# Kernel optimization log

Hardware: AMD Instinct MI355X
Metric: run time of the kernel (lower is better)

The kernel has to match this reference:

```python
import jax, jax.numpy as jnp
import numpy as np

# pywt db4 reconstruction low-pass (rec_lo) coefficients.
_H = np.array([
    0.23037781330885523, 0.7148465705525415, 0.6308807679295904,
    -0.02798376941698385, -0.18703481171888114, 0.030841381835986965,
    0.032883011666982945, -0.010597401784997278], dtype=np.float64)
# pywt dec_lo = _H[::-1]; conv (flipped) correlation kernel = dec_lo[::-1] = _H.
_FLO = _H
# dec_hi[k] = (-1)^(7-k) * _H[k]; correlation kernel = dec_hi[::-1] -> (-1)^k * _H[7-k].
_FHI = np.array([(-1.0) ** k * _H[7 - k] for k in range(8)])
_FILT = jnp.asarray(np.stack([_FLO, _FHI])[:, None, :], dtype=jnp.float32)  # [2,1,8]
_PAD = 7  # filter_len - 1
_LEVEL = 4


def _dwt_step(sig):
    """One pywt dwt level, mode='symmetric'. sig: [N, L] -> (cA, cD), each [N, (L+7)//2]."""
    # symmetric (half-sample) extension by filter_len-1 each side, drop first sample
    # so that stride-2 VALID correlation reproduces pywt's output phase/length.
    xp = jnp.pad(sig, ((0, 0), (_PAD, _PAD)), mode='symmetric')[:, 1:]
    out = jax.lax.conv_general_dilated(
        xp[:, None, :], _FILT, window_strides=(2,), padding='VALID',
        dimension_numbers=('NCH', 'OIH', 'NCH'))  # [N, 2, (L+7)//2]
    return out[:, 0, :], out[:, 1, :]


def setup_inputs() -> dict:
    key = jax.random.key(0)
    x = jax.random.normal(key, (64, 4096, 32), dtype=jnp.float32)  # [B, L, C]
    return {"x": x}


def reference(x):
    """Faithful batched version of pywt.wavedec(x[i,:,j], 'db4', 'symmetric', level=4).
    Returns tuple (cA4, cD4, cD3, cD2, cD1), each [B, C, scale_len]."""
    B, L, C = x.shape
    sig = jnp.transpose(x, (0, 2, 1)).reshape(B * C, L)
    details = []
    for _ in range(_LEVEL):
        sig, cd = _dwt_step(sig)
        details.append(cd)
    coeffs = [sig] + details[::-1]  # [cA_L, cD_L, ..., cD_1] like pywt.wavedec
    return tuple(c.reshape(B, C, c.shape[-1]) for c in coeffs)
```

## Files before the change

### kernel.cpp

```cpp
#include <hip/hip_runtime.h>


#define NT 256
#define NCHB 4

#define LPX 634
#define LP1 322
#define LP2 166
#define LP3 86
#define CDP1 314
#define CDP2 154
#define CDP3 82
#define CDP4 40
#define CAP4 40

#define L0C 4096
#define L1C 2051
#define L2C 1029
#define L3C 518
#define L4C 262
#define SC 2048

#define OFF_CD4 (SC * L4C)
#define OFF_CD3 (2 * SC * L4C)
#define OFF_CD2 (OFF_CD3 + SC * L3C)
#define OFF_CD1 (OFF_CD2 + SC * L2C)

__device__ __forceinline__ void filt8(
    const float w0, const float w1, const float w2, const float w3,
    const float w4, const float w5, const float w6, const float w7,
    float& a, float& d) {
    constexpr float FLO[8] = {
        0.23037781330885523f,  0.7148465705525415f,  0.6308807679295904f,
        -0.02798376941698385f, -0.18703481171888114f, 0.030841381835986965f,
        0.032883011666982945f, -0.010597401784997278f};
    constexpr float FHI[8] = {
        -0.010597401784997278f, -0.032883011666982945f, 0.030841381835986965f,
        0.18703481171888114f,  -0.02798376941698385f,  -0.6308807679295904f,
        0.7148465705525415f,   -0.23037781330885523f};
    float a0 = FLO[0] * w0;
    a0 = fmaf(FLO[1], w1, a0); a0 = fmaf(FLO[2], w2, a0); a0 = fmaf(FLO[3], w3, a0);
    float a1 = FLO[4] * w4;
    a1 = fmaf(FLO[5], w5, a1); a1 = fmaf(FLO[6], w6, a1); a1 = fmaf(FLO[7], w7, a1);
    a = a0 + a1;
    float d0 = FHI[0] * w0;
    d0 = fmaf(FHI[1], w1, d0); d0 = fmaf(FHI[2], w2, d0); d0 = fmaf(FHI[3], w3, d0);
    float d1 = FHI[4] * w4;
    d1 = fmaf(FHI[5], w5, d1); d1 = fmaf(FHI[6], w6, d1); d1 = fmaf(FHI[7], w7, d1);
    d = d0 + d1;
}

template <int R, bool MG, bool LAST>
__device__ __forceinline__ void level_run(
    const float* __restrict__ src, int PS, int srclo,
    float* __restrict__ dst, int PD, int DL,
    int lo, int hi,
    float* __restrict__ cdbuf, int CDP,
    float* __restrict__ cabuf,
    int c, int slot) {
    static_assert((R & 1) == 0, "R must be even");
    const int span = hi - lo;
    const int nrun = span / R;
    bool tail = false;
    int i0;
    if (slot < nrun) {
        i0 = lo + slot * R;
    } else if (slot == nrun && nrun * R < span) {
        i0 = lo + ((span - R) & ~1);
        tail = (span & 1) != 0;
    } else {
        return;
    }

    const float* rowb = src + c * PS;
    const float2* row2 = reinterpret_cast<const float2*>(rowb);
    const int p = i0 - (srclo >> 1);
    float2 f0 = row2[p], f1 = row2[p + 1], f2 = row2[p + 2];

    float* dbase = LAST ? nullptr : dst + c * PD;
    float* cdbase = cdbuf + c * CDP;
    float* cabase = LAST ? cabuf + c * CAP4 : nullptr;

    float ap = 0.f, dp = 0.f;
#pragma unroll
    for (int r = 0; r < R; ++r) {
        const float2 f3 = row2[p + 3 + r];
        const int i = i0 + r;
        float a, d;
        filt8(f0.x, f0.y, f1.x, f1.y, f2.x, f2.y, f3.x, f3.y, a, d);
        if (r & 1) {
            const int w = i - 1 - lo;
            if constexpr (!LAST)
                *reinterpret_cast<float2*>(dbase + w + 6) = make_float2(ap, a);
            else
                *reinterpret_cast<float2*>(cabase + w) = make_float2(ap, a);
            *reinterpret_cast<float2*>(cdbase + w) = make_float2(dp, d);
        } else {
            ap = a; dp = d;
        }
        if constexpr (MG && !LAST) {
            if (lo == 0 && i < 6) dbase[5 - i] = a;
            if (hi == DL && i >= DL - 7) dbase[(2 * DL - 1 - i) - lo + 6] = a;
        }
        f0 = f1; f1 = f2; f2 = f3;
    }
    if (tail) {
        const int i = hi - 1;
        const float* s = rowb + 6 - srclo;
        float a, d;
        filt8(s[2*i-6], s[2*i-5], s[2*i-4], s[2*i-3],
              s[2*i-2], s[2*i-1], s[2*i],   s[2*i+1], a, d);
        if constexpr (!LAST) {
            dbase[i - lo + 6] = a;
            if constexpr (MG) {
                if (hi == DL && i >= DL - 7) dbase[(2 * DL - 1 - i) - lo + 6] = a;
            }
        } else {
            cabase[i - lo] = a;
        }
        cdbase[i - lo] = d;
    }
}

__device__ __forceinline__ void dump_rows(
    const float* __restrict__ buf, int pitch, int bufLo,
    float* __restrict__ gbase, int rowLen, int ownLo, int ownHi, int tid) {
    const int span = ownHi - ownLo;
    const int n2 = span >> 1;
    const int off = ownLo - bufLo;
#pragma unroll
    for (int c2 = 0; c2 < NCHB; ++c2) {
        const float2* s2 = reinterpret_cast<const float2*>(buf + c2 * pitch + off);
        float* g = gbase + c2 * rowLen + ownLo;
        for (int k = tid; k < n2; k += NT) {
            const float2 v = s2[k];
            g[2 * k] = v.x;
            g[2 * k + 1] = v.y;
        }
        if ((span & 1) && tid == 0) g[span - 1] = buf[c2 * pitch + off + span - 1];
    }
}

template <bool MG>
__device__ __forceinline__ void cascade(
    const float* bx, float* b1, float* b2, float* b3,
    float* cd1, float* cd2, float* cd3, float* cd4, float* ca4,
    float* __restrict__ out, int sigB, int tile, int c, int slot, int tid,
    int lox, int lo1, int hi1, int lo2, int hi2, int lo3, int hi3,
    int lo4, int hi4) {
    const int o1lo = tile ? 264 * tile - 34 : 0;
    const int o1hi = (tile == 7) ? L1C : 264 * tile + 230;
    const int o2lo = tile ? 132 * tile - 10 : 0;
    const int o2hi = (tile == 7) ? L2C : 132 * tile + 122;
    const int o3lo = tile ? 66 * tile - 2 : 0;
    const int o3hi = (tile == 7) ? L3C : 66 * tile + 64;

    level_run<6, MG, false>(bx, LPX, lox, b1, LP1, L1C, lo1, hi1, cd1, CDP1,
                            nullptr, c, slot);
    __syncthreads();

    dump_rows(cd1, CDP1, lo1, out + OFF_CD1 + sigB * L1C, L1C, o1lo, o1hi, tid);
    level_run<4, MG, false>(b1, LP1, lo1, b2, LP2, L2C, lo2, hi2, cd2, CDP2,
                            nullptr, c, slot);
    __syncthreads();

    dump_rows(cd2, CDP2, lo2, out + OFF_CD2 + sigB * L2C, L2C, o2lo, o2hi, tid);
    level_run<2, MG, false>(b2, LP2, lo2, b3, LP3, L3C, lo3, hi3, cd3, CDP3,
                            nullptr, c, slot);
    __syncthreads();

    dump_rows(cd3, CDP3, lo3, out + OFF_CD3 + sigB * L3C, L3C, o3lo, o3hi, tid);
    level_run<2, MG, true>(b3, LP3, lo3, nullptr, 0, L4C, lo4, hi4, cd4, CDP4,
                           ca4, c, slot);
    __syncthreads();

    dump_rows(cd4, CDP4, lo4, out + OFF_CD4 + sigB * L4C, L4C, lo4, hi4, tid);
    dump_rows(ca4, CAP4, lo4, out + sigB * L4C, L4C, lo4, hi4, tid);
}

__global__ __launch_bounds__(NT, 5) void fused_dwt_kernel(
    const float* __restrict__ x, float* __restrict__ out) {
    __shared__ __align__(16) float bx[NCHB * LPX];
    __shared__ __align__(16) float b1[NCHB * LP1];
    __shared__ __align__(16) float b2[NCHB * LP2];
    __shared__ __align__(16) float b3[NCHB * LP3];
    __shared__ __align__(16) float cd1[NCHB * CDP1];
    __shared__ __align__(16) float cd2[NCHB * CDP2];
    __shared__ __align__(16) float cd3[NCHB * CDP3];
    __shared__ __align__(16) float cd4[NCHB * CDP4];
    __shared__ __align__(16) float ca4[NCHB * CAP4];

    const int bid = blockIdx.x;
    const int work = (bid & 7) * 512 + (bid >> 3);
    const int cg = work & 7;
    const int tile = (work >> 3) & 7;
    const int b = work >> 6;

    const int tid = threadIdx.x;
    const int c = tid & 3;
    const int slot = tid >> 2;
    const int c0 = cg * 4;
    const int sigB = b * 32 + c0;

    const int lo4 = 33 * tile, hi4 = min(L4C, lo4 + 33);
    const int lo3 = max(0, 2 * lo4 - 6), hi3 = min(L3C, 2 * hi4);
    const int lo2 = max(0, 2 * lo3 - 6), hi2 = min(L2C, 2 * hi3);
    const int lo1 = max(0, 2 * lo2 - 6), hi1 = min(L1C, 2 * hi2);
    const int lox = max(0, 2 * lo1 - 6), hix = min(L0C, 2 * hi1);

    const float* xb = x + b * (L0C * 32) + c0;
    const int npair = (hix - lox) >> 1;
    for (int q = tid; q < npair; q += NT) {
        const int j = q << 1;
        const int t = lox + j;
        const float4 va = *reinterpret_cast<const float4*>(xb + t * 32);
        const float4 vb = *reinterpret_cast<const float4*>(xb + t * 32 + 32);
        const float av[4] = {va.x, va.y, va.z, va.w};
        const float bv[4] = {vb.x, vb.y, vb.z, vb.w};
#pragma unroll
        for (int hh = 0; hh < NCHB; ++hh)
            *reinterpret_cast<float2*>(bx + hh * LPX + 6 + j) =
                make_float2(av[hh], bv[hh]);
        if (lox == 0 && t < 6) {
#pragma unroll
            for (int hh = 0; hh < NCHB; ++hh) {
                bx[hh * LPX + 5 - t] = av[hh];
                if (t + 1 < 6) bx[hh * LPX + 4 - t] = bv[hh];
            }
        }
        if (hix == L0C && t + 1 >= L0C - 7) {
#pragma unroll
            for (int hh = 0; hh < NCHB; ++hh) {
                if (t >= L0C - 7) bx[hh * LPX + (2 * L0C - 1 - t) - lox + 6] = av[hh];
                bx[hh * LPX + (2 * L0C - 2 - t) - lox + 6] = bv[hh];
            }
        }
    }
    __syncthreads();

    if (tile == 0 || tile == 7)
        cascade<true>(bx, b1, b2, b3, cd1, cd2, cd3, cd4, ca4, out, sigB, tile,
                      c, slot, tid, lox, lo1, hi1, lo2, hi2, lo3, hi3, lo4, hi4);
    else
        cascade<false>(bx, b1, b2, b3, cd1, cd2, cd3, cd4, ca4, out, sigB, tile,
                       c, slot, tid, lox, lo1, hi1, lo2, hi2, lo3, hi3, lo4, hi4);
}

extern "C" void kernel_launch(void* const* d_in, const int* in_sizes, int n_in,
                              void* d_out, int out_size, void* d_ws, size_t ws_size,
                              hipStream_t stream) {
    (void)in_sizes; (void)n_in; (void)d_ws; (void)ws_size; (void)out_size;
    const float* x = (const float*)d_in[0];
    float* out = (float*)d_out;
    fused_dwt_kernel<<<dim3(4096), dim3(NT), 0, stream>>>(x, out);
}
```

Before: 30.11 us.

## Split fused DWT into two kernels with global workspace for levels 3-4

```diff
diff --git a/kernel.cpp b/kernel.cpp
--- a/kernel.cpp
+++ b/kernel.cpp
@@ -3,16 +3,6 @@
 
 #define NT 256
 #define NCHB 4
-
-#define LPX 634
-#define LP1 322
-#define LP2 166
-#define LP3 86
-#define CDP1 314
-#define CDP2 154
-#define CDP3 82
-#define CDP4 40
-#define CAP4 40
 
 #define L0C 4096
 #define L1C 2051
@@ -20,11 +10,23 @@
 #define L3C 518
 #define L4C 262
 #define SC 2048
+#define WSL 1032
 
 #define OFF_CD4 (SC * L4C)
 #define OFF_CD3 (2 * SC * L4C)
 #define OFF_CD2 (OFF_CD3 + SC * L3C)
 #define OFF_CD1 (OFF_CD2 + SC * L2C)
+
+#define PX1 550
+#define PB1 278
+#define PD1 266
+#define PD2 130
+#define PA2 130
+#define PAS 1042
+#define PB3 534
+#define PD3 522
+#define PD4 266
+#define PA4 266
 
 __device__ __forceinline__ void filt8(
     const float w0, const float w1, const float w2, const float w3,
@@ -56,7 +58,7 @@
     float* __restrict__ dst, int PD, int DL,
     int lo, int hi,
     float* __restrict__ cdbuf, int CDP,
-    float* __restrict__ cabuf,
+    float* __restrict__ cabuf, int CAP,
     int c, int slot) {
     static_assert((R & 1) == 0, "R must be even");
     const int span = hi - lo;
@@ -79,7 +81,7 @@
 
     float* dbase = LAST ? nullptr : dst + c * PD;
     float* cdbase = cdbuf + c * CDP;
-    float* cabase = LAST ? cabuf + c * CAP4 : nullptr;
+    float* cabase = LAST ? cabuf + c * CAP : nullptr;
 
     float ap = 0.f, dp = 0.f;
 #pragma unroll
@@ -142,53 +144,35 @@
 }
 
 template <bool MG>
-__device__ __forceinline__ void cascade(
-    const float* bx, float* b1, float* b2, float* b3,
-    float* cd1, float* cd2, float* cd3, float* cd4, float* ca4,
-    float* __restrict__ out, int sigB, int tile, int c, int slot, int tid,
-    int lox, int lo1, int hi1, int lo2, int hi2, int lo3, int hi3,
-    int lo4, int hi4) {
-    const int o1lo = tile ? 264 * tile - 34 : 0;
-    const int o1hi = (tile == 7) ? L1C : 264 * tile + 230;
-    const int o2lo = tile ? 132 * tile - 10 : 0;
-    const int o2hi = (tile == 7) ? L2C : 132 * tile + 122;
-    const int o3lo = tile ? 66 * tile - 2 : 0;
-    const int o3hi = (tile == 7) ? L3C : 66 * tile + 64;
-
-    level_run<6, MG, false>(bx, LPX, lox, b1, LP1, L1C, lo1, hi1, cd1, CDP1,
-                            nullptr, c, slot);
-    __syncthreads();
-
-    dump_rows(cd1, CDP1, lo1, out + OFF_CD1 + sigB * L1C, L1C, o1lo, o1hi, tid);
-    level_run<4, MG, false>(b1, LP1, lo1, b2, LP2, L2C, lo2, hi2, cd2, CDP2,
-                            nullptr, c, slot);
-    __syncthreads();
-
-    dump_rows(cd2, CDP2, lo2, out + OFF_CD2 + sigB * L2C, L2C, o2lo, o2hi, tid);
-    level_run<2, MG, false>(b2, LP2, lo2, b3, LP3, L3C, lo3, hi3, cd3, CDP3,
-                            nullptr, c, slot);
-    __syncthreads();
-
-    dump_rows(cd3, CDP3, lo3, out + OFF_CD3 + sigB * L3C, L3C, o3lo, o3hi, tid);
-    level_run<2, MG, true>(b3, LP3, lo3, nullptr, 0, L4C, lo4, hi4, cd4, CDP4,
-                           ca4, c, slot);
-    __syncthreads();
-
-    dump_rows(cd4, CDP4, lo4, out + OFF_CD4 + sigB * L4C, L4C, lo4, hi4, tid);
-    dump_rows(ca4, CAP4, lo4, out + sigB * L4C, L4C, lo4, hi4, tid);
-}
-
-__global__ __launch_bounds__(NT, 5) void fused_dwt_kernel(
-    const float* __restrict__ x, float* __restrict__ out) {
-    __shared__ __align__(16) float bx[NCHB * LPX];
-    __shared__ __align__(16) float b1[NCHB * LP1];
-    __shared__ __align__(16) float b2[NCHB * LP2];
-    __shared__ __align__(16) float b3[NCHB * LP3];
-    __shared__ __align__(16) float cd1[NCHB * CDP1];
-    __shared__ __align__(16) float cd2[NCHB * CDP2];
-    __shared__ __align__(16) float cd3[NCHB * CDP3];
-    __shared__ __align__(16) float cd4[NCHB * CDP4];
-    __shared__ __align__(16) float ca4[NCHB * CAP4];
+__device__ __forceinline__ void k1_cascade(
+    const float* bx, float* b1, float* cd1, float* cd2, float* ca2,
+    float* __restrict__ out, float* __restrict__ ws,
+    int sigB, int tile, int c, int slot, int tid,
+    int lox, int lo1, int hi1, int lo2, int hi2) {
+    const int o1lo = tile ? 258 * tile : 0;
+    const int o1hi = (tile == 7) ? L1C : 258 * (tile + 1);
+
+    level_run<6, MG, false>(bx, PX1, lox, b1, PB1, L1C, lo1, hi1,
+                            cd1, PD1, nullptr, 0, c, slot);
+    __syncthreads();
+
+    dump_rows(cd1, PD1, lo1, out + OFF_CD1 + sigB * L1C, L1C, o1lo, o1hi, tid);
+    level_run<4, false, true>(b1, PB1, lo1, nullptr, 0, L2C, lo2, hi2,
+                              cd2, PD2, ca2, PA2, c, slot);
+    __syncthreads();
+
+    dump_rows(cd2, PD2, lo2, out + OFF_CD2 + sigB * L2C, L2C, lo2, hi2, tid);
+    dump_rows(ca2, PA2, lo2, ws + sigB * WSL, WSL, lo2, hi2, tid);
+}
+
+__global__ __launch_bounds__(NT) void dwt12_kernel(
+    const float* __restrict__ x, float* __restrict__ out,
+    float* __restrict__ ws) {
+    __shared__ __align__(16) float bx[NCHB * PX1];
+    __shared__ __align__(16) float b1[NCHB * PB1];
+    __shared__ __align__(16) float cd1[NCHB * PD1];
+    __shared__ __align__(16) float cd2[NCHB * PD2];
+    __shared__ __align__(16) float ca2[NCHB * PA2];
 
     const int bid = blockIdx.x;
     const int work = (bid & 7) * 512 + (bid >> 3);
@@ -202,9 +186,7 @@
     const int c0 = cg * 4;
     const int sigB = b * 32 + c0;
 
-    const int lo4 = 33 * tile, hi4 = min(L4C, lo4 + 33);
-    const int lo3 = max(0, 2 * lo4 - 6), hi3 = min(L3C, 2 * hi4);
-    const int lo2 = max(0, 2 * lo3 - 6), hi2 = min(L2C, 2 * hi3);
+    const int lo2 = 129 * tile, hi2 = min(L2C, lo2 + 129);
     const int lo1 = max(0, 2 * lo2 - 6), hi1 = min(L1C, 2 * hi2);
     const int lox = max(0, 2 * lo1 - 6), hix = min(L0C, 2 * hi1);
 
@@ -219,38 +201,97 @@
         const float bv[4] = {vb.x, vb.y, vb.z, vb.w};
 #pragma unroll
         for (int hh = 0; hh < NCHB; ++hh)
-            *reinterpret_cast<float2*>(bx + hh * LPX + 6 + j) =
+            *reinterpret_cast<float2*>(bx + hh * PX1 + 6 + j) =
                 make_float2(av[hh], bv[hh]);
         if (lox == 0 && t < 6) {
 #pragma unroll
             for (int hh = 0; hh < NCHB; ++hh) {
-                bx[hh * LPX + 5 - t] = av[hh];
-                if (t + 1 < 6) bx[hh * LPX + 4 - t] = bv[hh];
+                bx[hh * PX1 + 5 - t] = av[hh];
+                if (t + 1 < 6) bx[hh * PX1 + 4 - t] = bv[hh];
             }
         }
         if (hix == L0C && t + 1 >= L0C - 7) {
 #pragma unroll
             for (int hh = 0; hh < NCHB; ++hh) {
-                if (t >= L0C - 7) bx[hh * LPX + (2 * L0C - 1 - t) - lox + 6] = av[hh];
-                bx[hh * LPX + (2 * L0C - 2 - t) - lox + 6] = bv[hh];
+                if (t >= L0C - 7) bx[hh * PX1 + (2 * L0C - 1 - t) - lox + 6] = av[hh];
+                bx[hh * PX1 + (2 * L0C - 2 - t) - lox + 6] = bv[hh];
             }
         }
     }
     __syncthreads();
 
     if (tile == 0 || tile == 7)
-        cascade<true>(bx, b1, b2, b3, cd1, cd2, cd3, cd4, ca4, out, sigB, tile,
-                      c, slot, tid, lox, lo1, hi1, lo2, hi2, lo3, hi3, lo4, hi4);
+        k1_cascade<true>(bx, b1, cd1, cd2, ca2, out, ws, sigB, tile, c, slot,
+                         tid, lox, lo1, hi1, lo2, hi2);
     else
-        cascade<false>(bx, b1, b2, b3, cd1, cd2, cd3, cd4, ca4, out, sigB, tile,
-                       c, slot, tid, lox, lo1, hi1, lo2, hi2, lo3, hi3, lo4, hi4);
+        k1_cascade<false>(bx, b1, cd1, cd2, ca2, out, ws, sigB, tile, c, slot,
+                          tid, lox, lo1, hi1, lo2, hi2);
+}
+
+__global__ __launch_bounds__(NT) void dwt34_kernel(
+    const float* __restrict__ ws, float* __restrict__ out) {
+    __shared__ __align__(16) float bA[NCHB * PAS];
+    __shared__ __align__(16) float b3[NCHB * PB3];
+    __shared__ __align__(16) float cd3[NCHB * PD3];
+    __shared__ __align__(16) float cd4[NCHB * PD4];
+    __shared__ __align__(16) float ca4[NCHB * PA4];
+
+    const int bid = blockIdx.x;
+    const int work = (bid & 7) * 64 + (bid >> 3);
+    const int cg = work & 7;
+    const int b = work >> 3;
+
+    const int tid = threadIdx.x;
+    const int c = tid & 3;
+    const int slot = tid >> 2;
+    const int sigB = b * 32 + cg * 4;
+
+    const float* wbase = ws + sigB * WSL;
+#pragma unroll
+    for (int c2 = 0; c2 < NCHB; ++c2) {
+        const float2* s2 = reinterpret_cast<const float2*>(wbase + c2 * WSL);
+        float* row = bA + c2 * PAS;
+        for (int k = tid; k < 514; k += NT) {
+            const float2 v = s2[k];
+            const int t = 2 * k;
+            *reinterpret_cast<float2*>(row + t + 6) = v;
+            if (t < 6) {
+                row[5 - t] = v.x;
+                if (t + 1 < 6) row[4 - t] = v.y;
+            }
+            if (t + 1 >= L2C - 7) {
+                if (t >= L2C - 7) row[(2 * L2C - 1 - t) + 6] = v.x;
+                row[(2 * L2C - 2 - t) + 6] = v.y;
+            }
+        }
+        if (tid == 0) {
+            const float v = wbase[c2 * WSL + (L2C - 1)];
+            row[(L2C - 1) + 6] = v;
+            row[(2 * L2C - 1 - (L2C - 1)) + 6] = v;
+        }
+    }
+    __syncthreads();
+
+    level_run<10, true, false>(bA, PAS, 0, b3, PB3, L3C, 0, L3C,
+                               cd3, PD3, nullptr, 0, c, slot);
+    __syncthreads();
+
+    dump_rows(cd3, PD3, 0, out + OFF_CD3 + sigB * L3C, L3C, 0, L3C, tid);
+    level_run<6, false, true>(b3, PB3, 0, nullptr, 0, L4C, 0, L4C,
+                              cd4, PD4, ca4, PA4, c, slot);
+    __syncthreads();
+
+    dump_rows(cd4, PD4, 0, out + OFF_CD4 + sigB * L4C, L4C, 0, L4C, tid);
+    dump_rows(ca4, PA4, 0, out + sigB * L4C, L4C, 0, L4C, tid);
 }
 
 extern "C" void kernel_launch(void* const* d_in, const int* in_sizes, int n_in,
                               void* d_out, int out_size, void* d_ws, size_t ws_size,
                               hipStream_t stream) {
-    (void)in_sizes; (void)n_in; (void)d_ws; (void)ws_size; (void)out_size;
+    (void)in_sizes; (void)n_in; (void)ws_size; (void)out_size;
     const float* x = (const float*)d_in[0];
     float* out = (float*)d_out;
-    fused_dwt_kernel<<<dim3(4096), dim3(NT), 0, stream>>>(x, out);
-}
+    float* ws = (float*)d_ws;
+    dwt12_kernel<<<dim3(4096), dim3(NT), 0, stream>>>(x, out, ws);
+    dwt34_kernel<<<dim3(512), dim3(NT), 0, stream>>>(ws, out);
+}
```

Measured after the change: 33.92 us. +12.7%, slower.

## Split each DWT level into two halves to overlap levels across barriers

Applied to the files above, without the earlier changes.

```diff
diff --git a/kernel.cpp b/kernel.cpp
--- a/kernel.cpp
+++ b/kernel.cpp
@@ -25,6 +25,11 @@
 #define OFF_CD3 (2 * SC * L4C)
 #define OFF_CD2 (OFF_CD3 + SC * L3C)
 #define OFF_CD1 (OFF_CD2 + SC * L2C)
+
+#define K1A 154
+#define K2A 72
+#define K3A 32
+#define K4A 12
 
 __device__ __forceinline__ void filt8(
     const float w0, const float w1, const float w2, const float w3,
@@ -54,9 +59,9 @@
 __device__ __forceinline__ void level_run(
     const float* __restrict__ src, int PS, int srclo,
     float* __restrict__ dst, int PD, int DL,
-    int lo, int hi,
+    int lo, int hi, int loF,
     float* __restrict__ cdbuf, int CDP,
-    float* __restrict__ cabuf,
+    float* __restrict__ cabuf, int CAP,
     int c, int slot) {
     static_assert((R & 1) == 0, "R must be even");
     const int span = hi - lo;
@@ -79,7 +84,7 @@
 
     float* dbase = LAST ? nullptr : dst + c * PD;
     float* cdbase = cdbuf + c * CDP;
-    float* cabase = LAST ? cabuf + c * CAP4 : nullptr;
+    float* cabase = LAST ? cabuf + c * CAP : nullptr;
 
     float ap = 0.f, dp = 0.f;
 #pragma unroll
@@ -89,7 +94,7 @@
         float a, d;
         filt8(f0.x, f0.y, f1.x, f1.y, f2.x, f2.y, f3.x, f3.y, a, d);
         if (r & 1) {
-            const int w = i - 1 - lo;
+            const int w = i - 1 - loF;
             if constexpr (!LAST)
                 *reinterpret_cast<float2*>(dbase + w + 6) = make_float2(ap, a);
             else
@@ -99,8 +104,8 @@
             ap = a; dp = d;
         }
         if constexpr (MG && !LAST) {
-            if (lo == 0 && i < 6) dbase[5 - i] = a;
-            if (hi == DL && i >= DL - 7) dbase[(2 * DL - 1 - i) - lo + 6] = a;
+            if (loF == 0 && i < 6) dbase[5 - i] = a;
+            if (hi == DL && i >= DL - 7) dbase[(2 * DL - 1 - i) - loF + 6] = a;
         }
         f0 = f1; f1 = f2; f2 = f3;
     }
@@ -111,14 +116,14 @@
         filt8(s[2*i-6], s[2*i-5], s[2*i-4], s[2*i-3],
               s[2*i-2], s[2*i-1], s[2*i],   s[2*i+1], a, d);
         if constexpr (!LAST) {
-            dbase[i - lo + 6] = a;
+            dbase[i - loF + 6] = a;
             if constexpr (MG) {
-                if (hi == DL && i >= DL - 7) dbase[(2 * DL - 1 - i) - lo + 6] = a;
+                if (hi == DL && i >= DL - 7) dbase[(2 * DL - 1 - i) - loF + 6] = a;
             }
         } else {
-            cabase[i - lo] = a;
-        }
-        cdbase[i - lo] = d;
+            cabase[i - loF] = a;
+        }
+        cdbase[i - loF] = d;
     }
 }
 
@@ -155,23 +160,33 @@
     const int o3lo = tile ? 66 * tile - 2 : 0;
     const int o3hi = (tile == 7) ? L3C : 66 * tile + 64;
 
-    level_run<6, MG, false>(bx, LPX, lox, b1, LP1, L1C, lo1, hi1, cd1, CDP1,
-                            nullptr, c, slot);
+    level_run<4, MG, false>(bx, LPX, lox, b1, LP1, L1C, lo1, lo1 + K1A, lo1,
+                            cd1, CDP1, nullptr, 0, c, slot);
+    __syncthreads();
+
+    level_run<4, MG, false>(bx, LPX, lox, b1, LP1, L1C, lo1 + K1A, hi1, lo1,
+                            cd1, CDP1, nullptr, 0, c, slot);
+    level_run<2, MG, false>(b1, LP1, lo1, b2, LP2, L2C, lo2, lo2 + K2A, lo2,
+                            cd2, CDP2, nullptr, 0, c, slot);
     __syncthreads();
 
     dump_rows(cd1, CDP1, lo1, out + OFF_CD1 + sigB * L1C, L1C, o1lo, o1hi, tid);
-    level_run<4, MG, false>(b1, LP1, lo1, b2, LP2, L2C, lo2, hi2, cd2, CDP2,
-                            nullptr, c, slot);
+    level_run<2, MG, false>(b1, LP1, lo1, b2, LP2, L2C, lo2 + K2A, hi2, lo2,
+                            cd2, CDP2, nullptr, 0, c, slot);
+    level_run<2, MG, false>(b2, LP2, lo2, b3, LP3, L3C, lo3, lo3 + K3A, lo3,
+                            cd3, CDP3, nullptr, 0, c, slot);
     __syncthreads();
 
     dump_rows(cd2, CDP2, lo2, out + OFF_CD2 + sigB * L2C, L2C, o2lo, o2hi, tid);
-    level_run<2, MG, false>(b2, LP2, lo2, b3, LP3, L3C, lo3, hi3, cd3, CDP3,
-                            nullptr, c, slot);
+    level_run<2, MG, false>(b2, LP2, lo2, b3, LP3, L3C, lo3 + K3A, hi3, lo3,
+                            cd3, CDP3, nullptr, 0, c, slot);
+    level_run<2, false, true>(b3, LP3, lo3, nullptr, 0, L4C, lo4, lo4 + K4A, lo4,
+                              cd4, CDP4, ca4, CAP4, c, slot);
     __syncthreads();
 
     dump_rows(cd3, CDP3, lo3, out + OFF_CD3 + sigB * L3C, L3C, o3lo, o3hi, tid);
-    level_run<2, MG, true>(b3, LP3, lo3, nullptr, 0, L4C, lo4, hi4, cd4, CDP4,
-                           ca4, c, slot);
+    level_run<2, false, true>(b3, LP3, lo3, nullptr, 0, L4C, lo4 + K4A, hi4, lo4,
+                              cd4, CDP4, ca4, CAP4, c, slot);
     __syncthreads();
 
     dump_rows(cd4, CDP4, lo4, out + OFF_CD4 + sigB * L4C, L4C, lo4, hi4, tid);
```

Result: slower. 32.32 us (+7.4%).

## Compose two DWT levels into 22-tap stride-4 filters to skip intermediate stages

Applied to the files above, without the earlier changes.

```diff
diff --git a/kernel.cpp b/kernel.cpp
--- a/kernel.cpp
+++ b/kernel.cpp
@@ -5,14 +5,12 @@
 #define NCHB 4
 
 #define LPX 634
-#define LP1 322
-#define LP2 166
-#define LP3 86
-#define CDP1 314
-#define CDP2 154
-#define CDP3 82
-#define CDP4 40
-#define CAP4 40
+#define LB2 166
+#define CDP1 266
+#define CDP2 134
+#define CDP3 70
+#define CDP4 34
+#define CAP4 34
 
 #define L0C 4096
 #define L1C 2051
@@ -26,128 +24,174 @@
 #define OFF_CD2 (OFF_CD3 + SC * L3C)
 #define OFF_CD1 (OFF_CD2 + SC * L2C)
 
-__device__ __forceinline__ void filt8(
-    const float w0, const float w1, const float w2, const float w3,
-    const float w4, const float w5, const float w6, const float w7,
-    float& a, float& d) {
-    constexpr float FLO[8] = {
+constexpr double DLO[8] = {
+    0.23037781330885523,  0.7148465705525415,  0.6308807679295904,
+    -0.02798376941698385, -0.18703481171888114, 0.030841381835986965,
+    0.032883011666982945, -0.010597401784997278};
+constexpr double DHI[8] = {
+    -0.010597401784997278, -0.032883011666982945, 0.030841381835986965,
+    0.18703481171888114,  -0.02798376941698385,  -0.6308807679295904,
+    0.7148465705525415,   -0.23037781330885523};
+
+struct E22 { float a[22]; float d[22]; };
+constexpr E22 make_e22() {
+    E22 e{};
+    double da[22] = {}, dd[22] = {};
+    for (int m = 0; m < 8; ++m)
+        for (int k = 0; k < 8; ++k) {
+            da[2 * m + k] += DLO[m] * DLO[k];
+            dd[2 * m + k] += DHI[m] * DLO[k];
+        }
+    for (int u = 0; u < 22; ++u) { e.a[u] = (float)da[u]; e.d[u] = (float)dd[u]; }
+    return e;
+}
+
+__device__ __forceinline__ float dot8lo(const float* __restrict__ w) {
+    constexpr float F[8] = {
         0.23037781330885523f,  0.7148465705525415f,  0.6308807679295904f,
         -0.02798376941698385f, -0.18703481171888114f, 0.030841381835986965f,
         0.032883011666982945f, -0.010597401784997278f};
-    constexpr float FHI[8] = {
+    float s0 = F[0] * w[0];
+    s0 = fmaf(F[1], w[1], s0); s0 = fmaf(F[2], w[2], s0); s0 = fmaf(F[3], w[3], s0);
+    float s1 = F[4] * w[4];
+    s1 = fmaf(F[5], w[5], s1); s1 = fmaf(F[6], w[6], s1); s1 = fmaf(F[7], w[7], s1);
+    return s0 + s1;
+}
+__device__ __forceinline__ float dot8hi(const float* __restrict__ w) {
+    constexpr float F[8] = {
         -0.010597401784997278f, -0.032883011666982945f, 0.030841381835986965f,
         0.18703481171888114f,  -0.02798376941698385f,  -0.6308807679295904f,
         0.7148465705525415f,   -0.23037781330885523f};
-    float a0 = FLO[0] * w0;
-    a0 = fmaf(FLO[1], w1, a0); a0 = fmaf(FLO[2], w2, a0); a0 = fmaf(FLO[3], w3, a0);
-    float a1 = FLO[4] * w4;
-    a1 = fmaf(FLO[5], w5, a1); a1 = fmaf(FLO[6], w6, a1); a1 = fmaf(FLO[7], w7, a1);
-    a = a0 + a1;
-    float d0 = FHI[0] * w0;
-    d0 = fmaf(FHI[1], w1, d0); d0 = fmaf(FHI[2], w2, d0); d0 = fmaf(FHI[3], w3, d0);
-    float d1 = FHI[4] * w4;
-    d1 = fmaf(FHI[5], w5, d1); d1 = fmaf(FHI[6], w6, d1); d1 = fmaf(FHI[7], w7, d1);
-    d = d0 + d1;
-}
-
-template <int R, bool MG, bool LAST>
-__device__ __forceinline__ void level_run(
+    float s0 = F[0] * w[0];
+    s0 = fmaf(F[1], w[1], s0); s0 = fmaf(F[2], w[2], s0); s0 = fmaf(F[3], w[3], s0);
+    float s1 = F[4] * w[4];
+    s1 = fmaf(F[5], w[5], s1); s1 = fmaf(F[6], w[6], s1); s1 = fmaf(F[7], w[7], s1);
+    return s0 + s1;
+}
+
+template <bool WA, bool WD>
+__device__ __forceinline__ void dot22t(const float* __restrict__ w, float& a, float& d) {
+    constexpr E22 E = make_e22();
+    float a0 = 0.f, a1 = 0.f, d0 = 0.f, d1 = 0.f;
+#pragma unroll
+    for (int u = 0; u < 22; u += 2) {
+        if constexpr (WA) a0 = fmaf(E.a[u], w[u], a0);
+        if constexpr (WD) d0 = fmaf(E.d[u], w[u], d0);
+    }
+#pragma unroll
+    for (int u = 1; u < 22; u += 2) {
+        if constexpr (WA) a1 = fmaf(E.a[u], w[u], a1);
+        if constexpr (WD) d1 = fmaf(E.d[u], w[u], d1);
+    }
+    if constexpr (WA) a = a0 + a1;
+    if constexpr (WD) d = d0 + d1;
+}
+
+template <int R>
+__device__ __forceinline__ void run8d(
     const float* __restrict__ src, int PS, int srclo,
-    float* __restrict__ dst, int PD, int DL,
     int lo, int hi,
-    float* __restrict__ cdbuf, int CDP,
-    float* __restrict__ cabuf,
+    float* __restrict__ dbuf, int DP, int obase,
     int c, int slot) {
-    static_assert((R & 1) == 0, "R must be even");
-    const int span = hi - lo;
-    const int nrun = span / R;
-    bool tail = false;
-    int i0;
-    if (slot < nrun) {
-        i0 = lo + slot * R;
-    } else if (slot == nrun && nrun * R < span) {
-        i0 = lo + ((span - R) & ~1);
-        tail = (span & 1) != 0;
-    } else {
-        return;
-    }
-
-    const float* rowb = src + c * PS;
-    const float2* row2 = reinterpret_cast<const float2*>(rowb);
+    int i0 = lo + slot * R;
+    if (i0 >= hi) return;
+    if (i0 > hi - R) i0 = hi - R;
+    const float2* row2 = reinterpret_cast<const float2*>(src + c * PS);
     const int p = i0 - (srclo >> 1);
-    float2 f0 = row2[p], f1 = row2[p + 1], f2 = row2[p + 2];
-
-    float* dbase = LAST ? nullptr : dst + c * PD;
-    float* cdbase = cdbuf + c * CDP;
-    float* cabase = LAST ? cabuf + c * CAP4 : nullptr;
-
-    float ap = 0.f, dp = 0.f;
+    float w[2 * R + 6];
+#pragma unroll
+    for (int j = 0; j < R + 3; ++j) {
+        const float2 v = row2[p + j];
+        w[2 * j] = v.x; w[2 * j + 1] = v.y;
+    }
+    float* drow = dbuf + c * DP - obase;
+#pragma unroll
+    for (int r = 0; r < R; ++r) drow[i0 + r] = dot8hi(&w[2 * r]);
+}
+
+template <int R, bool WITH_A>
+__device__ __forceinline__ void run22s(
+    const float* __restrict__ src, int PS, int srclo,
+    int lo, int hi,
+    float* __restrict__ dbuf, int DP,
+    float* __restrict__ abuf, int AP, int obase,
+    int c, int slot) {
+    int i0 = lo + slot * R;
+    if (i0 >= hi) return;
+    if (i0 > hi - R) i0 = hi - R;
+    const float2* row2 = reinterpret_cast<const float2*>(src + c * PS);
+    const int p = 2 * i0 - 6 - (srclo >> 1);
+    float w[4 * R + 18];
+#pragma unroll
+    for (int j = 0; j < 2 * R + 9; ++j) {
+        const float2 v = row2[p + j];
+        w[2 * j] = v.x; w[2 * j + 1] = v.y;
+    }
+    float* drow = dbuf + c * DP - obase;
 #pragma unroll
     for (int r = 0; r < R; ++r) {
-        const float2 f3 = row2[p + 3 + r];
+        float a, d;
+        dot22t<WITH_A, true>(&w[4 * r], a, d);
+        drow[i0 + r] = d;
+        if constexpr (WITH_A) (abuf + c * AP - obase)[i0 + r] = a;
+    }
+}
+
+template <int R, bool MG>
+__device__ __forceinline__ void run22w(
+    const float* __restrict__ src, int PS, int srclo,
+    int lo, int hi,
+    float* __restrict__ b2, int wlo,
+    int c, int slot) {
+    int i0 = lo + slot * R;
+    if (i0 >= hi) return;
+    if (i0 > hi - R) i0 = hi - R;
+    const float2* row2 = reinterpret_cast<const float2*>(src + c * PS);
+    const int p = 2 * i0 - 6 - (srclo >> 1);
+    float w[4 * R + 18];
+#pragma unroll
+    for (int j = 0; j < 2 * R + 9; ++j) {
+        const float2 v = row2[p + j];
+        w[2 * j] = v.x; w[2 * j + 1] = v.y;
+    }
+    float* wr = b2 + c * LB2;
+#pragma unroll
+    for (int r = 0; r < R; ++r) {
+        float a, dummy;
+        dot22t<true, false>(&w[4 * r], a, dummy);
         const int i = i0 + r;
-        float a, d;
-        filt8(f0.x, f0.y, f1.x, f1.y, f2.x, f2.y, f3.x, f3.y, a, d);
-        if (r & 1) {
-            const int w = i - 1 - lo;
-            if constexpr (!LAST)
-                *reinterpret_cast<float2*>(dbase + w + 6) = make_float2(ap, a);
-            else
-                *reinterpret_cast<float2*>(cabase + w) = make_float2(ap, a);
-            *reinterpret_cast<float2*>(cdbase + w) = make_float2(dp, d);
-        } else {
-            ap = a; dp = d;
-        }
-        if constexpr (MG && !LAST) {
-            if (lo == 0 && i < 6) dbase[5 - i] = a;
-            if (hi == DL && i >= DL - 7) dbase[(2 * DL - 1 - i) - lo + 6] = a;
-        }
-        f0 = f1; f1 = f2; f2 = f3;
-    }
-    if (tail) {
-        const int i = hi - 1;
-        const float* s = rowb + 6 - srclo;
-        float a, d;
-        filt8(s[2*i-6], s[2*i-5], s[2*i-4], s[2*i-3],
-              s[2*i-2], s[2*i-1], s[2*i],   s[2*i+1], a, d);
-        if constexpr (!LAST) {
-            dbase[i - lo + 6] = a;
-            if constexpr (MG) {
-                if (hi == DL && i >= DL - 7) dbase[(2 * DL - 1 - i) - lo + 6] = a;
-            }
-        } else {
-            cabase[i - lo] = a;
-        }
-        cdbase[i - lo] = d;
+        wr[i - wlo + 6] = a;
+        if constexpr (MG) {
+            if (wlo == 0 && i < 6) wr[5 - i] = a;
+            if (i >= L2C - 7) wr[(2 * L2C - 1 - i) - wlo + 6] = a;
+        }
     }
 }
 
 __device__ __forceinline__ void dump_rows(
-    const float* __restrict__ buf, int pitch, int bufLo,
+    const float* __restrict__ buf, int pitch,
     float* __restrict__ gbase, int rowLen, int ownLo, int ownHi, int tid) {
     const int span = ownHi - ownLo;
     const int n2 = span >> 1;
-    const int off = ownLo - bufLo;
 #pragma unroll
     for (int c2 = 0; c2 < NCHB; ++c2) {
-        const float2* s2 = reinterpret_cast<const float2*>(buf + c2 * pitch + off);
+        const float2* s2 = reinterpret_cast<const float2*>(buf + c2 * pitch);
         float* g = gbase + c2 * rowLen + ownLo;
         for (int k = tid; k < n2; k += NT) {
             const float2 v = s2[k];
             g[2 * k] = v.x;
             g[2 * k + 1] = v.y;
         }
-        if ((span & 1) && tid == 0) g[span - 1] = buf[c2 * pitch + off + span - 1];
+        if ((span & 1) && tid == 0) g[span - 1] = buf[c2 * pitch + span - 1];
     }
 }
 
 template <bool MG>
 __device__ __forceinline__ void cascade(
-    const float* bx, float* b1, float* b2, float* b3,
+    const float* bx, float* b2,
     float* cd1, float* cd2, float* cd3, float* cd4, float* ca4,
     float* __restrict__ out, int sigB, int tile, int c, int slot, int tid,
-    int lox, int lo1, int hi1, int lo2, int hi2, int lo3, int hi3,
-    int lo4, int hi4) {
+    int lox, int lo2, int hi2, int lo4, int hi4) {
     const int o1lo = tile ? 264 * tile - 34 : 0;
     const int o1hi = (tile == 7) ? L1C : 264 * tile + 230;
     const int o2lo = tile ? 132 * tile - 10 : 0;
@@ -155,35 +199,93 @@
     const int o3lo = tile ? 66 * tile - 2 : 0;
     const int o3hi = (tile == 7) ? L3C : 66 * tile + 64;
 
-    level_run<6, MG, false>(bx, LPX, lox, b1, LP1, L1C, lo1, hi1, cd1, CDP1,
-                            nullptr, c, slot);
+    const int d2lo = MG ? max(o2lo, 3) : o2lo;
+    const int d2hi = MG ? min(o2hi, 1025) : o2hi;
+    const int a2lo = MG ? max(lo2, 3) : lo2;
+    const int a2hi = MG ? min(hi2, 1025) : hi2;
+    const int c4lo = MG ? max(lo4, 3) : lo4;
+    const int c4hi = MG ? min(hi4, 259) : hi4;
+
+    run8d<6>(bx, LPX, lox, o1lo, o1hi, cd1, CDP1, o1lo, c, slot);
+    run22s<3, false>(bx, LPX, lox, d2lo, d2hi, cd2, CDP2, nullptr, 0, o2lo,
+                     c, (slot + 44) & 63);
+    run22w<3, MG>(bx, LPX, lox, a2lo, a2hi, b2, lo2, c, (slot + 32) & 63);
+    if (MG && slot == 19) {
+        const float* xr = bx + c * LPX + 6 - lox;
+        float* wr = b2 + c * LB2;
+        float* cd2row = cd2 + c * CDP2 - o2lo;
+        const int ilo = (lo2 == 0) ? 0 : 1025;
+        const int ihi = (lo2 == 0) ? 3 : L2C;
+        for (int i = ilo; i < ihi; ++i) {
+            float a = 0.f, d = 0.f;
+#pragma unroll
+            for (int m = 0; m < 8; ++m) {
+                int j = 2 * i - 6 + m;
+                j = (j < 0) ? -1 - j : ((j >= L1C) ? 2 * L1C - 1 - j : j);
+                const float s = dot8lo(xr + 2 * j - 6);
+                constexpr float FL[8] = {
+                    0.23037781330885523f,  0.7148465705525415f,  0.6308807679295904f,
+                    -0.02798376941698385f, -0.18703481171888114f, 0.030841381835986965f,
+                    0.032883011666982945f, -0.010597401784997278f};
+                constexpr float FH[8] = {
+                    -0.010597401784997278f, -0.032883011666982945f, 0.030841381835986965f,
+                    0.18703481171888114f,  -0.02798376941698385f,  -0.6308807679295904f,
+                    0.7148465705525415f,   -0.23037781330885523f};
+                a = fmaf(FL[m], s, a);
+                d = fmaf(FH[m], s, d);
+            }
+            wr[i - lo2 + 6] = a;
+            if (lo2 == 0 && i < 6) wr[5 - i] = a;
+            if (i >= L2C - 7) wr[(2 * L2C - 1 - i) - lo2 + 6] = a;
+            if (i >= o2lo && i < o2hi) cd2row[i] = d;
+        }
+    }
     __syncthreads();
 
-    dump_rows(cd1, CDP1, lo1, out + OFF_CD1 + sigB * L1C, L1C, o1lo, o1hi, tid);
-    level_run<4, MG, false>(b1, LP1, lo1, b2, LP2, L2C, lo2, hi2, cd2, CDP2,
-                            nullptr, c, slot);
+    dump_rows(cd1, CDP1, out + OFF_CD1 + sigB * L1C, L1C, o1lo, o1hi, tid);
+    dump_rows(cd2, CDP2, out + OFF_CD2 + sigB * L2C, L2C, o2lo, o2hi, tid);
+    run8d<2>(b2, LB2, lo2, o3lo, o3hi, cd3, CDP3, o3lo, c, slot);
+    run22s<2, true>(b2, LB2, lo2, c4lo, c4hi, cd4, CDP4, ca4, CAP4, lo4,
+                    c, (slot + 34) & 63);
+    if (MG && slot == 63) {
+        const float* a2 = b2 + c * LB2 + 6 - lo2;
+        float* ca4row = ca4 + c * CAP4 - lo4;
+        float* cd4row = cd4 + c * CDP4 - lo4;
+        const int ilo = (lo4 == 0) ? 0 : 259;
+        const int ihi = (lo4 == 0) ? 3 : L4C;
+        for (int i = ilo; i < ihi; ++i) {
+            float a = 0.f, d = 0.f;
+#pragma unroll
+            for (int m = 0; m < 8; ++m) {
+                int j = 2 * i - 6 + m;
+                j = (j < 0) ? -1 - j : ((j >= L3C) ? 2 * L3C - 1 - j : j);
+                const float s = dot8lo(a2 + 2 * j - 6);
+                constexpr float FL[8] = {
+                    0.23037781330885523f,  0.7148465705525415f,  0.6308807679295904f,
+                    -0.02798376941698385f, -0.18703481171888114f, 0.030841381835986965f,
+                    0.032883011666982945f, -0.010597401784997278f};
+                constexpr float FH[8] = {
+                    -0.010597401784997278f, -0.032883011666982945f, 0.030841381835986965f,
+                    0.18703481171888114f,  -0.02798376941698385f,  -0.6308807679295904f,
+                    0.7148465705525415f,   -0.23037781330885523f};
+                a = fmaf(FL[m], s, a);
+                d = fmaf(FH[m], s, d);
+            }
+            ca4row[i] = a;
+            cd4row[i] = d;
+        }
+    }
     __syncthreads();
 
-    dump_rows(cd2, CDP2, lo2, out + OFF_CD2 + sigB * L2C, L2C, o2lo, o2hi, tid);
-    level_run<2, MG, false>(b2, LP2, lo2, b3, LP3, L3C, lo3, hi3, cd3, CDP3,
-                            nullptr, c, slot);
-    __syncthreads();
-
-    dump_rows(cd3, CDP3, lo3, out + OFF_CD3 + sigB * L3C, L3C, o3lo, o3hi, tid);
-    level_run<2, MG, true>(b3, LP3, lo3, nullptr, 0, L4C, lo4, hi4, cd4, CDP4,
-                           ca4, c, slot);
-    __syncthreads();
-
-    dump_rows(cd4, CDP4, lo4, out + OFF_CD4 + sigB * L4C, L4C, lo4, hi4, tid);
-    dump_rows(ca4, CAP4, lo4, out + sigB * L4C, L4C, lo4, hi4, tid);
-}
-
-__global__ __launch_bounds__(NT, 5) void fused_dwt_kernel(
+    dump_rows(cd3, CDP3, out + OFF_CD3 + sigB * L3C, L3C, o3lo, o3hi, tid);
+    dump_rows(cd4, CDP4, out + OFF_CD4 + sigB * L4C, L4C, lo4, hi4, tid);
+    dump_rows(ca4, CAP4, out + sigB * L4C, L4C, lo4, hi4, tid);
+}
+
+__global__ __launch_bounds__(NT) void fused_dwt_kernel(
     const float* __restrict__ x, float* __restrict__ out) {
     __shared__ __align__(16) float bx[NCHB * LPX];
-    __shared__ __align__(16) float b1[NCHB * LP1];
-    __shared__ __align__(16) float b2[NCHB * LP2];
-    __shared__ __align__(16) float b3[NCHB * LP3];
+    __shared__ __align__(16) float b2[NCHB * LB2];
     __shared__ __align__(16) float cd1[NCHB * CDP1];
     __shared__ __align__(16) float cd2[NCHB * CDP2];
     __shared__ __align__(16) float cd3[NCHB * CDP3];
@@ -239,11 +341,11 @@
     __syncthreads();
 
     if (tile == 0 || tile == 7)
-        cascade<true>(bx, b1, b2, b3, cd1, cd2, cd3, cd4, ca4, out, sigB, tile,
-                      c, slot, tid, lox, lo1, hi1, lo2, hi2, lo3, hi3, lo4, hi4);
+        cascade<true>(bx, b2, cd1, cd2, cd3, cd4, ca4, out, sigB, tile,
+                      c, slot, tid, lox, lo2, hi2, lo4, hi4);
     else
-        cascade<false>(bx, b1, b2, b3, cd1, cd2, cd3, cd4, ca4, out, sigB, tile,
-                       c, slot, tid, lox, lo1, hi1, lo2, hi2, lo3, hi3, lo4, hi4);
+        cascade<false>(bx, b2, cd1, cd2, cd3, cd4, ca4, out, sigB, tile,
+                       c, slot, tid, lox, lo2, hi2, lo4, hi4);
 }
 
 extern "C" void kernel_launch(void* const* d_in, const int* in_sizes, int n_in,
```

Measured after the change: 33.05 us. 9.8% more time.
